# Performance work log

Hardware: AMD Instinct MI355X
Metric: run time of the kernel (lower is better)

The kernel has to match this reference:

```python
import jax, jax.numpy as jnp
import numpy as np

EPS_LN = 1e-5

def _ln(x, g, b):
    m = x.mean(-1, keepdims=True)
    v = jnp.var(x, axis=-1, keepdims=True)
    return (x - m) * jax.lax.rsqrt(v + EPS_LN) * g + b


def _forward(x, edge_attr, lin0_w, lin0_b, enn_w1, enn_b1, enn_g1, enn_b1n,
             enn_w2, enn_b2, enn_g2, enn_b2n, conv_bias,
             gru_w_ih, gru_w_hh, gru_b_ih, gru_b_hh,
             lstm_w_ih, lstm_w_hh, lstm_b_ih, lstm_b_hh,
             lin1_w, lin1_b, lin1_g, lin1_bn, lin2_w, lin2_b,
             edge_index, target_index, target_class):
    N = x.shape[0]
    D = lin0_w.shape[0]
    src, dst = edge_index[0], edge_index[1]

    out = jax.nn.relu(x @ lin0_w.T + lin0_b)            # [N, D]
    h = out                                             # GRU hidden state

    # edge NN -> per-edge weight matrix [E, D, D] (edge_attr constant across iters)
    e1 = jax.nn.relu(_ln(edge_attr @ enn_w1.T + enn_b1, enn_g1, enn_b1n))
    ew = _ln(e1 @ enn_w2.T + enn_b2, enn_g2, enn_b2n).reshape(-1, D, D)

    counts = jnp.clip(jax.ops.segment_sum(jnp.ones_like(dst, jnp.float32), dst, num_segments=N), 1.0)[:, None]

    for _ in range(3):
        msg = jnp.einsum('ed,edo->eo', out[src], ew)     # per-edge matmul
        agg = jax.ops.segment_sum(msg, dst, num_segments=N) / counts  # scatter-mean
        m = jax.nn.relu(agg + conv_bias)
        # GRU cell (seq len 1)
        gx = m @ gru_w_ih.T + gru_b_ih
        gh = h @ gru_w_hh.T + gru_b_hh
        xr, xz, xn = jnp.split(gx, 3, axis=-1)
        hr, hz, hn = jnp.split(gh, 3, axis=-1)
        r = jax.nn.sigmoid(xr + hr)
        z = jax.nn.sigmoid(xz + hz)
        n = jnp.tanh(xn + r * hn)
        h = (1.0 - z) * n + z * h
        out = h

    # Set2Set with batch_index = arange(N) (each node is its own set), 3 steps
    idx = jnp.arange(N)
    hl = jnp.zeros((N, D), x.dtype)
    cl = jnp.zeros((N, D), x.dtype)
    q_star = jnp.zeros((N, 2 * D), x.dtype)
    for _ in range(3):
        g = q_star @ lstm_w_ih.T + lstm_b_ih + hl @ lstm_w_hh.T + lstm_b_hh
        gi, gf, gg, go = jnp.split(g, 4, axis=-1)
        cl = jax.nn.sigmoid(gf) * cl + jax.nn.sigmoid(gi) * jnp.tanh(gg)
        hl = jax.nn.sigmoid(go) * jnp.tanh(cl)
        q = hl
        e = (out * q[idx]).sum(-1, keepdims=True)
        emax = jax.ops.segment_max(e, idx, num_segments=N)
        a = jnp.exp(e - emax[idx])
        a = a / (jax.ops.segment_sum(a, idx, num_segments=N)[idx] + 1e-16)
        r_pool = jax.ops.segment_sum(a * out, idx, num_segments=N)
        q_star = jnp.concatenate([q, r_pool], axis=-1)

    a0, a1 = target_index[0], target_index[1]
    cat = jnp.concatenate([out[a0], out[a1], q_star[a0], q_star[a1]], axis=-1)  # [P, 6D]
    p = jax.nn.relu(_ln(cat @ lin1_w.T + lin1_b, lin1_g, lin1_bn))
    p = p @ lin2_w.T + lin2_b                           # [P, 8]
    return jnp.take_along_axis(p, target_class[:, None], axis=1)[:, 0]


def setup_inputs() -> dict:
    N, E, P, F, D = 10000, 20000, 15000, 16, 64
    ks = iter(jax.random.split(jax.random.key(0), 40))
    def nrm(shape, s=0.1):
        return jax.random.normal(next(ks), shape, jnp.float32) * s
    return {
        'x': jax.random.normal(next(ks), (N, F), jnp.float32),
        'edge_attr': jax.random.normal(next(ks), (E, 4), jnp.float32),
        'lin0_w': nrm((D, F)), 'lin0_b': jnp.zeros((D,), jnp.float32),
        'enn_w1': nrm((128, 4)), 'enn_b1': jnp.zeros((128,), jnp.float32),
        'enn_g1': jnp.ones((128,), jnp.float32), 'enn_b1n': jnp.zeros((128,), jnp.float32),
        'enn_w2': nrm((D * D, 128), 0.05), 'enn_b2': jnp.zeros((D * D,), jnp.float32),
        'enn_g2': jnp.ones((D * D,), jnp.float32), 'enn_b2n': jnp.zeros((D * D,), jnp.float32),
        'conv_bias': jnp.zeros((D,), jnp.float32),
        'gru_w_ih': nrm((3 * D, D)), 'gru_w_hh': nrm((3 * D, D)),
        'gru_b_ih': jnp.zeros((3 * D,), jnp.float32), 'gru_b_hh': jnp.zeros((3 * D,), jnp.float32),
        'lstm_w_ih': nrm((4 * D, 2 * D)), 'lstm_w_hh': nrm((4 * D, D)),
        'lstm_b_ih': jnp.zeros((4 * D,), jnp.float32), 'lstm_b_hh': jnp.zeros((4 * D,), jnp.float32),
        'lin1_w': nrm((D, 6 * D)), 'lin1_b': jnp.zeros((D,), jnp.float32),
        'lin1_g': jnp.ones((D,), jnp.float32), 'lin1_bn': jnp.zeros((D,), jnp.float32),
        'lin2_w': nrm((8, D)), 'lin2_b': jnp.zeros((8,), jnp.float32),
        'edge_index': jax.random.randint(next(ks), (2, E), 0, N),
        'target_index': jax.random.randint(next(ks), (2, P), 0, N),
        'target_class': jax.random.randint(next(ks), (P,), 0, 8),
    }


def reference(x, edge_attr, lin0_w, lin0_b, enn_w1, enn_b1, enn_g1, enn_b1n,
              enn_w2, enn_b2, enn_g2, enn_b2n, conv_bias,
              gru_w_ih, gru_w_hh, gru_b_ih, gru_b_hh,
              lstm_w_ih, lstm_w_hh, lstm_b_ih, lstm_b_hh,
              lin1_w, lin1_b, lin1_g, lin1_bn, lin2_w, lin2_b,
              edge_index, target_index, target_class):
    return _forward(x, edge_attr, lin0_w, lin0_b, enn_w1, enn_b1, enn_g1, enn_b1n,
                    enn_w2, enn_b2, enn_g2, enn_b2n, conv_bias,
                    gru_w_ih, gru_w_hh, gru_b_ih, gru_b_hh,
                    lstm_w_ih, lstm_w_hh, lstm_b_ih, lstm_b_hh,
                    lin1_w, lin1_b, lin1_g, lin1_bn, lin2_w, lin2_b,
                    edge_index, target_index, target_class)
```

## Files before the change

### kernel.cpp

```cpp
#include <hip/hip_runtime.h>
#include <hip/hip_bf16.h>

#define EPS_LN 1e-5f

typedef __attribute__((ext_vector_type(8))) short bf16x8;
typedef __attribute__((ext_vector_type(4))) float f32x4;

__device__ __forceinline__ float dot4(float4 a, float4 b) {
    return a.x * b.x + a.y * b.y + a.z * b.z + a.w * b.w;
}
__device__ __forceinline__ float sigmoidf_(float x) { return 1.0f / (1.0f + expf(-x)); }

__device__ __forceinline__ float bfu2f(unsigned short u) {
    unsigned v = ((unsigned)u) << 16;
    float f;
    __builtin_memcpy(&f, &v, 4);
    return f;
}
__device__ __forceinline__ unsigned short f2bfu(float f) {
    __hip_bfloat16 h = __float2bfloat16(f);
    unsigned short u;
    __builtin_memcpy(&u, &h, 2);
    return u;
}
__device__ __forceinline__ unsigned pack2bf(float a, float b) {
    return (unsigned)f2bfu(a) | ((unsigned)f2bfu(b) << 16);
}

__global__ void init_kernel(const float* __restrict__ x, const float* __restrict__ w,
                            const float* __restrict__ b, float* __restrict__ h,
                            const int* __restrict__ ei, float* __restrict__ counts,
                            int N, int E) {
    int id = blockIdx.x * blockDim.x + threadIdx.x;
    if (id < N * 64) {
        int n = id >> 6, o = id & 63;
        const float* xr = x + n * 16;
        const float* wr = w + o * 16;
        float acc = b[o];
#pragma unroll
        for (int k = 0; k < 16; k++) acc += xr[k] * wr[k];
        h[id] = fmaxf(acc, 0.0f);
    }
    if (id < E) atomicAdd(&counts[ei[E + id]], 1.0f);
}

__global__ __launch_bounds__(128) void edge_nn1_kernel(
    const float* __restrict__ ea, const float* __restrict__ w1, const float* __restrict__ b1,
    const float* __restrict__ g1, const float* __restrict__ b1n,
    unsigned short* __restrict__ e1h, unsigned short* __restrict__ e1l, int E) {
    int e = blockIdx.x, j = threadIdx.x;
    float a0 = ea[e * 4 + 0], a1 = ea[e * 4 + 1], a2 = ea[e * 4 + 2], a3 = ea[e * 4 + 3];
    const float* wr = w1 + j * 4;
    float z = b1[j] + a0 * wr[0] + a1 * wr[1] + a2 * wr[2] + a3 * wr[3];
    float s = z, s2 = z * z;
#pragma unroll
    for (int m = 32; m >= 1; m >>= 1) { s += __shfl_xor(s, m); s2 += __shfl_xor(s2, m); }
    __shared__ float ls[2], ls2[2];
    int wv = j >> 6;
    if ((j & 63) == 0) { ls[wv] = s; ls2[wv] = s2; }
    __syncthreads();
    float S = ls[0] + ls[1], S2 = ls2[0] + ls2[1];
    float mu = S * (1.0f / 128.0f);
    float var = fmaxf(S2 * (1.0f / 128.0f) - mu * mu, 0.0f);
    float inv = rsqrtf(var + EPS_LN);
    float v = fmaxf((z - mu) * inv * g1[j] + b1n[j], 0.0f);
    unsigned short hi = f2bfu(v);
    unsigned short lo = f2bfu(v - bfu2f(hi));
    e1h[e * 128 + j] = hi;
    e1l[e * 128 + j] = lo;
}

__global__ __launch_bounds__(128) void mpart_kernel(const float* __restrict__ w2,
                                                    const float* __restrict__ b2,
                                                    const float* __restrict__ g2,
                                                    unsigned short* __restrict__ w2g,
                                                    float* __restrict__ b2g,
                                                    float* __restrict__ pMT, float* __restrict__ pv,
                                                    float* __restrict__ pcw, float* __restrict__ psb,
                                                    float* __restrict__ pc) {
    __shared__ float wL[16][128];
    __shared__ float b2L[16];
    int t = threadIdx.x, b = blockIdx.x;
#pragma unroll
    for (int i = 0; i < 16; i++) {
        int idx = t + i * 128;
        wL[idx >> 7][idx & 127] = w2[(size_t)(b * 16 + (idx >> 7)) * 128 + (idx & 127)];
    }
    if (t < 16) b2L[t] = b2[b * 16 + t];
    __syncthreads();
#pragma unroll
    for (int o = 0; o < 16; o++) {
        int row = b * 16 + o;
        w2g[(size_t)row * 128 + t] = f2bfu(wL[o][t] * g2[row]);
    }
    if (t < 16) b2g[b * 16 + t] = b2L[t] * g2[b * 16 + t];
    int j = t;
    float wj[16];
#pragma unroll
    for (int o = 0; o < 16; o++) wj[o] = wL[o][j];
    float pvj = 0.f, pcwj = 0.f;
#pragma unroll
    for (int o = 0; o < 16; o++) { pvj += wj[o] * b2L[o]; pcwj += wj[o]; }
    for (int i4 = 0; i4 < 32; i4++) {
        float4 a = {0.f, 0.f, 0.f, 0.f};
#pragma unroll
        for (int o = 0; o < 16; o++) {
            float4 w4 = *(const float4*)&wL[o][i4 * 4];
            a.x += wj[o] * w4.x; a.y += wj[o] * w4.y;
            a.z += wj[o] * w4.z; a.w += wj[o] * w4.w;
        }
        *(float4*)&pMT[((size_t)b * 128 + j) * 128 + i4 * 4] = a;
    }
    pv[b * 128 + j] = pvj;
    pcw[b * 128 + j] = pcwj;
    if (t == 0) {
        float sb = 0.f, cc = 0.f;
#pragma unroll
        for (int o = 0; o < 16; o++) { sb += b2L[o]; cc += b2L[o] * b2L[o]; }
        psb[b] = sb;
        pc[b] = cc;
    }
}

__global__ __launch_bounds__(256) void mreduce_kernel(const float* __restrict__ pMT,
                                                      const float* __restrict__ pv,
                                                      const float* __restrict__ pcw,
                                                      const float* __restrict__ psb,
                                                      const float* __restrict__ pc,
                                                      unsigned short* __restrict__ mb,
                                                      float* __restrict__ varr,
                                                      float* __restrict__ cw,
                                                      float* __restrict__ sbc) {
    int fid = blockIdx.x * 256 + threadIdx.x;
    float s = 0.f;
    int j = fid >> 7, i = fid & 127;
    for (int b = 0; b < 256; b++) s += pMT[((size_t)b * 128 + j) * 128 + i];
    mb[fid] = f2bfu(s);
    if (fid < 128) {
        float sv = 0.f, sc = 0.f;
        for (int b = 0; b < 256; b++) { sv += pv[b * 128 + fid]; sc += pcw[b * 128 + fid]; }
        varr[fid] = sv;
        cw[fid] = sc;
    }
    if (fid == 0) {
        float sb = 0.f, cc = 0.f;
        for (int b = 0; b < 256; b++) { sb += psb[b]; cc += pc[b]; }
        sbc[0] = sb;
        sbc[1] = cc;
    }
}

__global__ __launch_bounds__(256) void stats_kernel(
    const unsigned short* __restrict__ e1h, const unsigned short* __restrict__ e1l,
    const unsigned short* __restrict__ mb, const float* __restrict__ cw,
    const float* __restrict__ varr, const float* __restrict__ sbc,
    float* __restrict__ stats, int E) {
    __shared__ __align__(16) unsigned char smem[65536];
    const int t = threadIdx.x;
    const int eb = blockIdx.x * 64;
#pragma unroll
    for (int r = 0; r < 4; r++) {
        int idx = t + r * 256;
        int row = idx >> 4, kseg = idx & 15;
        int er = eb + row;
        if (er >= E) er = E - 1;
        uint4 vh = *(const uint4*)&e1h[(size_t)er * 128 + kseg * 8];
        uint4 vl = *(const uint4*)&e1l[(size_t)er * 128 + kseg * 8];
        int off = row * 256 + ((kseg * 16) ^ ((row & 7) << 4));
        *(uint4*)(smem + off) = vh;
        *(uint4*)(smem + 16384 + off) = vl;
    }
#pragma unroll
    for (int r = 0; r < 8; r++) {
        int idx = t + r * 256;
        int row = idx >> 4, kseg = idx & 15;
        uint4 v = *(const uint4*)&mb[(size_t)row * 128 + kseg * 8];
        *(uint4*)(smem + 32768 + row * 256 + ((kseg * 16) ^ ((row & 7) << 4))) = v;
    }
    __syncthreads();
    const int w = t >> 6, lane = t & 63;
    const int wrow = w * 16;
    const int r16 = lane & 15, kg = lane >> 4;
    f32x4 tacc[8];
#pragma unroll
    for (int nj = 0; nj < 8; nj++) tacc[nj] = (f32x4){0.f, 0.f, 0.f, 0.f};
#pragma unroll
    for (int ks = 0; ks < 4; ks++) {
        int arow = wrow + r16;
        int koff = ks * 64 + kg * 16;
        bf16x8 ah = *(const bf16x8*)(smem + arow * 256 + (koff ^ ((arow & 7) << 4)));
        bf16x8 al = *(const bf16x8*)(smem + 16384 + arow * 256 + (koff ^ ((arow & 7) << 4)));
#pragma unroll
        for (int nj = 0; nj < 8; nj++) {
            int brow = nj * 16 + r16;
            bf16x8 bf = *(const bf16x8*)(smem + 32768 + brow * 256 + (koff ^ ((brow & 7) << 4)));
            tacc[nj] = __builtin_amdgcn_mfma_f32_16x16x32_bf16(ah, bf, tacc[nj], 0, 0, 0);
            tacc[nj] = __builtin_amdgcn_mfma_f32_16x16x32_bf16(al, bf, tacc[nj], 0, 0, 0);
        }
    }
    __syncthreads();
#pragma unroll
    for (int nj = 0; nj < 8; nj++)
#pragma unroll
        for (int r = 0; r < 4; r++) {
            int row = wrow + kg * 4 + r, col = nj * 16 + r16;
            *(float*)(smem + 32768 + row * 512 + col * 4) = tacc[nj][r];
        }
    __syncthreads();
    int el = t >> 2, q = t & 3;
    float s2p = 0.f, sp = 0.f, svp = 0.f;
    for (int kk = 0; kk < 32; kk++) {
        int k = q * 32 + kk;
        int boff = el * 256 + ((2 * k) ^ ((el & 7) << 4));
        float e1v = bfu2f(*(const unsigned short*)(smem + boff)) +
                    bfu2f(*(const unsigned short*)(smem + 16384 + boff));
        float tv = *(const float*)(smem + 32768 + el * 512 + k * 4);
        s2p += tv * e1v;
        sp += e1v * cw[k];
        svp += e1v * varr[k];
    }
    s2p += __shfl_xor(s2p, 1); s2p += __shfl_xor(s2p, 2);
    sp += __shfl_xor(sp, 1);   sp += __shfl_xor(sp, 2);
    svp += __shfl_xor(svp, 1); svp += __shfl_xor(svp, 2);
    if (q == 0) {
        int e = eb + el;
        if (e < E) {
            float S = sp + sbc[0];
            float S2 = s2p + 2.f * svp + sbc[1];
            float mu = S * (1.0f / 4096.0f);
            float var = fmaxf(S2 * (1.0f / 4096.0f) - mu * mu, 0.0f);
            float inv = rsqrtf(var + EPS_LN);
            stats[e * 2 + 0] = inv;
            stats[e * 2 + 1] = mu * inv;
        }
    }
}

__global__ __launch_bounds__(256) void zgemm_final(
    const unsigned short* __restrict__ e1h, const unsigned short* __restrict__ e1l,
    const unsigned short* __restrict__ w2g, const float* __restrict__ b2g,
    const float* __restrict__ g2, const float* __restrict__ b2n,
    const float* __restrict__ stats, unsigned short* __restrict__ zT, int E) {
    __shared__ __align__(16) unsigned char smem[65536];
    const int t = threadIdx.x;
    const int eb = blockIdx.y * 64;
    const int cb = blockIdx.x * 128;
    const int o0 = blockIdx.x * 2;
#pragma unroll
    for (int r = 0; r < 4; r++) {
        int idx = t + r * 256;
        int row = idx >> 4, kseg = idx & 15;
        int er = eb + row;
        if (er >= E) er = E - 1;
        uint4 vh = *(const uint4*)&e1h[(size_t)er * 128 + kseg * 8];
        uint4 vl = *(const uint4*)&e1l[(size_t)er * 128 + kseg * 8];
        int off = row * 256 + ((kseg * 16) ^ ((row & 7) << 4));
        *(uint4*)(smem + off) = vh;
        *(uint4*)(smem + 16384 + off) = vl;
    }
#pragma unroll
    for (int r = 0; r < 8; r++) {
        int idx = t + r * 256;
        int j = idx >> 4, kseg = idx & 15;
        int srcrow = ((j & 63) << 6) + o0 + (j >> 6);
        uint4 v = *(const uint4*)&w2g[(size_t)srcrow * 128 + kseg * 8];
        *(uint4*)(smem + 32768 + j * 256 + ((kseg * 16) ^ ((j & 7) << 4))) = v;
    }
    __syncthreads();
    const int w = t >> 6, lane = t & 63;
    const int wrow = (w >> 1) * 32, wcol = (w & 1) * 64;
    const int r16 = lane & 15, kg = lane >> 4;

    bf16x8 bfrag[4][4];
#pragma unroll
    for (int nj = 0; nj < 4; nj++)
#pragma unroll
        for (int ks = 0; ks < 4; ks++) {
            int row = wcol + nj * 16 + r16;
            int koff = ks * 64 + kg * 16;
            bfrag[nj][ks] = *(const bf16x8*)(smem + 32768 + row * 256 + (koff ^ ((row & 7) << 4)));
        }
    f32x4 acc[2][4];
#pragma unroll
    for (int mi = 0; mi < 2; mi++)
#pragma unroll
        for (int nj = 0; nj < 4; nj++) acc[mi][nj] = (f32x4){0.f, 0.f, 0.f, 0.f};
#pragma unroll
    for (int pass = 0; pass < 2; pass++) {
        int abase = pass * 16384;
#pragma unroll
        for (int ks = 0; ks < 4; ks++) {
            bf16x8 afrag[2];
#pragma unroll
            for (int mi = 0; mi < 2; mi++) {
                int row = wrow + mi * 16 + r16;
                int koff = ks * 64 + kg * 16;
                afrag[mi] = *(const bf16x8*)(smem + abase + row * 256 + (koff ^ ((row & 7) << 4)));
            }
#pragma unroll
            for (int mi = 0; mi < 2; mi++)
#pragma unroll
                for (int nj = 0; nj < 4; nj++)
                    acc[mi][nj] = __builtin_amdgcn_mfma_f32_16x16x32_bf16(
                        afrag[mi], bfrag[nj][ks], acc[mi][nj], 0, 0, 0);
        }
    }
    float bg[4], gg[4], bn[4];
#pragma unroll
    for (int nj = 0; nj < 4; nj++) {
        int j = wcol + nj * 16 + r16;
        int sj = ((j & 63) << 6) + o0 + (j >> 6);
        bg[nj] = b2g[sj];
        gg[nj] = g2[sj];
        bn[nj] = b2n[sj];
    }
    __syncthreads();
#pragma unroll
    for (int mi = 0; mi < 2; mi++)
#pragma unroll
        for (int r = 0; r < 4; r++) {
            int rowl = wrow + mi * 16 + kg * 4 + r;
            int eg = eb + rowl;
            if (eg >= E) eg = E - 1;
            float inv = stats[eg * 2 + 0], miv = stats[eg * 2 + 1];
#pragma unroll
            for (int nj = 0; nj < 4; nj++) {
                int j = wcol + nj * 16 + r16;
                float v = inv * (acc[mi][nj][r] + bg[nj]) - miv * gg[nj] + bn[nj];
                *(unsigned short*)(smem + rowl * 272 + j * 2) = f2bfu(v);
            }
        }
    __syncthreads();
#pragma unroll
    for (int r = 0; r < 4; r++) {
        int idx = t + r * 256;
        int row = idx >> 4, seg = idx & 15;
        if (eb + row < E) {
            uint4 v = *(const uint4*)(smem + row * 272 + seg * 16);
            *(uint4*)&zT[(size_t)(eb + row) * 4096 + cb + seg * 8] = v;
        }
    }
}

__global__ __launch_bounds__(256) void msg_kernel(const unsigned short* __restrict__ zT,
                                                  const float* __restrict__ h,
                                                  const int* __restrict__ ei,
                                                  float* __restrict__ agg, int E) {
    int t = threadIdx.x;
    int el = t >> 6, o = t & 63;
    int e = blockIdx.x * 4 + el;
    __shared__ float sL[4][64];
    int src = ei[e];
    int dstn = ei[E + e];
    sL[el][o] = h[src * 64 + o];
    __syncthreads();
    float acc = 0.f;
    const uint4* zp = (const uint4*)(zT + (size_t)e * 4096 + o * 64);
#pragma unroll
    for (int q = 0; q < 8; q++) {
        uint4 v = zp[q];
        const float* hp = &sL[el][q * 8];
        acc += __uint_as_float(v.x << 16) * hp[0] + __uint_as_float(v.x & 0xffff0000u) * hp[1];
        acc += __uint_as_float(v.y << 16) * hp[2] + __uint_as_float(v.y & 0xffff0000u) * hp[3];
        acc += __uint_as_float(v.z << 16) * hp[4] + __uint_as_float(v.z & 0xffff0000u) * hp[5];
        acc += __uint_as_float(v.w << 16) * hp[6] + __uint_as_float(v.w & 0xffff0000u) * hp[7];
    }
    atomicAdd(&agg[(size_t)dstn * 64 + o], acc);
}

__global__ __launch_bounds__(192) void gru_kernel(
    const float* __restrict__ agg, const float* __restrict__ counts, const float* __restrict__ cbias,
    const float* __restrict__ wih, const float* __restrict__ whh,
    const float* __restrict__ bih, const float* __restrict__ bhh, float* __restrict__ h, int N) {
    int t = threadIdx.x;
    int nb = blockIdx.x * 8;
    __shared__ __align__(16) float mL[8][64], hL[8][64], gxL[8][192], ghL[8][192];
    for (int idx = t; idx < 512; idx += 192) {
        int n = idx >> 6, k = idx & 63;
        int node = nb + n;
        float cnt = fmaxf(counts[node], 1.0f);
        mL[n][k] = fmaxf(agg[node * 64 + k] / cnt + cbias[k], 0.0f);
        hL[n][k] = h[node * 64 + k];
    }
    __syncthreads();
    {
        int j = t;
        float ax[8], ah[8];
#pragma unroll
        for (int n = 0; n < 8; n++) { ax[n] = 0.f; ah[n] = 0.f; }
        const float4* wi = (const float4*)(wih + j * 64);
        const float4* wh = (const float4*)(whh + j * 64);
#pragma unroll 4
        for (int k4 = 0; k4 < 16; k4++) {
            float4 wiv = wi[k4], whv = wh[k4];
#pragma unroll
            for (int n = 0; n < 8; n++) {
                ax[n] += dot4(wiv, *(const float4*)&mL[n][k4 * 4]);
                ah[n] += dot4(whv, *(const float4*)&hL[n][k4 * 4]);
            }
        }
        float bi = bih[j], bh = bhh[j];
#pragma unroll
        for (int n = 0; n < 8; n++) { gxL[n][j] = ax[n] + bi; ghL[n][j] = ah[n] + bh; }
    }
    __syncthreads();
    for (int idx = t; idx < 512; idx += 192) {
        int n = idx >> 6, k = idx & 63;
        int node = nb + n;
        float r = sigmoidf_(gxL[n][k] + ghL[n][k]);
        float zz = sigmoidf_(gxL[n][64 + k] + ghL[n][64 + k]);
        float nn = tanhf(gxL[n][128 + k] + r * ghL[n][128 + k]);
        h[node * 64 + k] = (1.0f - zz) * nn + zz * hL[n][k];
    }
}

__global__ __launch_bounds__(256) void coutprep_kernel(
    const float* __restrict__ h, const float* __restrict__ wih, const float* __restrict__ whh,
    const float* __restrict__ bih, const float* __restrict__ bhh,
    float* __restrict__ cout, float* __restrict__ wc,
    float* __restrict__ hl, float* __restrict__ cl, int N) {
    int t = threadIdx.x, nb = blockIdx.x * 8;
    __shared__ __align__(16) float oL[8][64];
    for (int idx = t; idx < 512; idx += 256) {
        int n = idx >> 6, k = idx & 63;
        oL[n][k] = h[(nb + n) * 64 + k];
    }
    __syncthreads();
    {
        float acc[8];
#pragma unroll
        for (int n = 0; n < 8; n++) acc[n] = 0.f;
        const float* wr = wih + t * 128 + 64;
#pragma unroll 4
        for (int k4 = 0; k4 < 16; k4++) {
            float4 w4 = *(const float4*)&wr[k4 * 4];
#pragma unroll
            for (int n = 0; n < 8; n++) acc[n] += dot4(w4, *(const float4*)&oL[n][k4 * 4]);
        }
#pragma unroll
        for (int n = 0; n < 8; n++) cout[(size_t)(nb + n) * 256 + t] = acc[n];
    }
    if (blockIdx.x < 64) {
        int id = blockIdx.x * 256 + t;
        int j = id >> 6, k = id & 63;
        wc[id] = wih[j * 128 + k] + whh[id];
    }
    if (t < 64) {
        float gi = bih[t] + bhh[t];
        float gg = bih[128 + t] + bhh[128 + t];
        float go = bih[192 + t] + bhh[192 + t];
        float c0 = sigmoidf_(gi) * tanhf(gg);
        float h0 = sigmoidf_(go) * tanhf(c0);
#pragma unroll
        for (int n = 0; n < 8; n++) {
            cl[(nb + n) * 64 + t] = c0;
            hl[(nb + n) * 64 + t] = h0;
        }
    }
}

__global__ __launch_bounds__(256) void lstm_step_kernel(const float* __restrict__ wc,
                                                        const float* __restrict__ bih,
                                                        const float* __restrict__ bhh,
                                                        const float* __restrict__ cout,
                                                        float* __restrict__ hl,
                                                        float* __restrict__ cl, int N) {
    int t = threadIdx.x, nb = blockIdx.x * 8;
    __shared__ __align__(16) float hlL[8][64];
    __shared__ float gL[8][256];
    for (int idx = t; idx < 512; idx += 256) {
        int n = idx >> 6, k = idx & 63;
        hlL[n][k] = hl[(nb + n) * 64 + k];
    }
    __syncthreads();
    {
        float acc[8];
#pragma unroll
        for (int n = 0; n < 8; n++) acc[n] = 0.f;
        const float4* w4p = (const float4*)(wc + t * 64);
#pragma unroll 4
        for (int k4 = 0; k4 < 16; k4++) {
            float4 w4 = w4p[k4];
#pragma unroll
            for (int n = 0; n < 8; n++) acc[n] += dot4(w4, *(const float4*)&hlL[n][k4 * 4]);
        }
        float bs = bih[t] + bhh[t];
#pragma unroll
        for (int n = 0; n < 8; n++) gL[n][t] = acc[n] + cout[(size_t)(nb + n) * 256 + t] + bs;
    }
    __syncthreads();
    for (int idx = t; idx < 512; idx += 256) {
        int n = idx >> 6, k = idx & 63;
        int node = nb + n;
        float gi = gL[n][k], gf = gL[n][64 + k], gg = gL[n][128 + k], go = gL[n][192 + k];
        float c = sigmoidf_(gf) * cl[node * 64 + k] + sigmoidf_(gi) * tanhf(gg);
        cl[node * 64 + k] = c;
        hl[node * 64 + k] = sigmoidf_(go) * tanhf(c);
    }
}

__global__ __launch_bounds__(256) void head_kernel(
    const float* __restrict__ h, const float* __restrict__ hl, const int* __restrict__ ti,
    const int* __restrict__ tc, const float* __restrict__ w1, const float* __restrict__ b1,
    const float* __restrict__ g1, const float* __restrict__ bn1, const float* __restrict__ w2,
    const float* __restrict__ b2, float* __restrict__ out, int P) {
    __shared__ uint2 w1q[6144];
    __shared__ float catL[4][384];
    int t = threadIdx.x;
    const float4* w1f4 = (const float4*)w1;
#pragma unroll
    for (int i = 0; i < 24; i++) {
        int f = t + i * 256;
        float4 v = w1f4[f];
        int j = f / 96, k4 = f - j * 96;
        w1q[k4 * 64 + j] = make_uint2(pack2bf(v.x, v.y), pack2bf(v.z, v.w));
    }
    int j = t & 63, pl = t >> 6;
    float b1j = b1[j], g1j = g1[j], bnj = bn1[j];
    __syncthreads();

    for (int pb = blockIdx.x * 4; pb < P; pb += gridDim.x * 4) {
#pragma unroll
        for (int i = 0; i < 6; i++) {
            int idx = t + i * 256;
            int p = idx / 384, kk = idx - p * 384;
            int pair = pb + p;
            if (pair >= P) pair = P - 1;
            int a0 = ti[pair], a1 = ti[P + pair];
            int s = kk >> 6, k = kk & 63;
            float v;
            if (s == 0 || s == 3) v = h[a0 * 64 + k];
            else if (s == 1 || s == 5) v = h[a1 * 64 + k];
            else if (s == 2) v = hl[a0 * 64 + k];
            else v = hl[a1 * 64 + k];
            catL[p][kk] = v;
        }
        __syncthreads();
        int pair = pb + pl;
        float acc = b1j;
#pragma unroll 8
        for (int k4 = 0; k4 < 96; k4++) {
            uint2 wv = w1q[k4 * 64 + j];
            float4 c = *(const float4*)&catL[pl][k4 * 4];
            acc += __uint_as_float(wv.x << 16) * c.x + __uint_as_float(wv.x & 0xffff0000u) * c.y;
            acc += __uint_as_float(wv.y << 16) * c.z + __uint_as_float(wv.y & 0xffff0000u) * c.w;
        }
        float s1 = acc, s2v = acc * acc;
#pragma unroll
        for (int m = 32; m >= 1; m >>= 1) { s1 += __shfl_xor(s1, m); s2v += __shfl_xor(s2v, m); }
        float mu = s1 * (1.0f / 64.0f);
        float var = fmaxf(s2v * (1.0f / 64.0f) - mu * mu, 0.0f);
        float p1 = fmaxf((acc - mu) * rsqrtf(var + EPS_LN) * g1j + bnj, 0.0f);
        int cls = tc[pair < P ? pair : P - 1];
        float part = p1 * w2[cls * 64 + j];
#pragma unroll
        for (int m = 32; m >= 1; m >>= 1) part += __shfl_xor(part, m);
        if (j == 0 && pair < P) out[pair] = part + b2[cls];
        __syncthreads();
    }
}

extern "C" void kernel_launch(void* const* d_in, const int* in_sizes, int n_in,
                              void* d_out, int out_size, void* d_ws, size_t ws_size,
                              hipStream_t stream) {
    const float* x = (const float*)d_in[0];
    const float* edge_attr = (const float*)d_in[1];
    const float* lin0_w = (const float*)d_in[2];
    const float* lin0_b = (const float*)d_in[3];
    const float* enn_w1 = (const float*)d_in[4];
    const float* enn_b1 = (const float*)d_in[5];
    const float* enn_g1 = (const float*)d_in[6];
    const float* enn_b1n = (const float*)d_in[7];
    const float* enn_w2 = (const float*)d_in[8];
    const float* enn_b2 = (const float*)d_in[9];
    const float* enn_g2 = (const float*)d_in[10];
    const float* enn_b2n = (const float*)d_in[11];
    const float* conv_bias = (const float*)d_in[12];
    const float* gru_w_ih = (const float*)d_in[13];
    const float* gru_w_hh = (const float*)d_in[14];
    const float* gru_b_ih = (const float*)d_in[15];
    const float* gru_b_hh = (const float*)d_in[16];
    const float* lstm_w_ih = (const float*)d_in[17];
    const float* lstm_w_hh = (const float*)d_in[18];
    const float* lstm_b_ih = (const float*)d_in[19];
    const float* lstm_b_hh = (const float*)d_in[20];
    const float* lin1_w = (const float*)d_in[21];
    const float* lin1_b = (const float*)d_in[22];
    const float* lin1_g = (const float*)d_in[23];
    const float* lin1_bn = (const float*)d_in[24];
    const float* lin2_w = (const float*)d_in[25];
    const float* lin2_b = (const float*)d_in[26];
    const int* edge_index = (const int*)d_in[27];
    const int* target_index = (const int*)d_in[28];
    const int* target_class = (const int*)d_in[29];

    const int N = in_sizes[0] / 16;
    const int E = in_sizes[27] / 2;
    const int P = in_sizes[29];

    size_t off = 0;
    auto carve = [&](size_t bytes) {
        void* p = (char*)d_ws + off;
        off += (bytes + 255) & ~(size_t)255;
        return p;
    };
    unsigned short* zbuf = (unsigned short*)carve((size_t)E * 4096 * 2);
    unsigned short* e1h = (unsigned short*)carve((size_t)E * 128 * 2);
    unsigned short* e1l = (unsigned short*)carve((size_t)E * 128 * 2);
    unsigned short* w2g = (unsigned short*)carve((size_t)4096 * 128 * 2);
    float* b2g = (float*)carve((size_t)4096 * 4);
    float* hbuf = (float*)carve((size_t)N * 64 * 4);
    float* counts = (float*)carve((size_t)N * 4 + (size_t)3 * N * 64 * 4);
    float* agg0 = counts + N;
    float* agg1 = agg0 + (size_t)N * 64;
    float* agg2 = agg1 + (size_t)N * 64;
    float* hl = (float*)carve((size_t)N * 64 * 4);
    float* cl = (float*)carve((size_t)N * 64 * 4);
    float* cout_b = (float*)carve((size_t)N * 256 * 4);
    float* wc = (float*)carve((size_t)256 * 64 * 4);
    float* stats = (float*)carve((size_t)E * 2 * 4);
    unsigned short* mb = (unsigned short*)carve((size_t)128 * 128 * 2);
    float* varr = (float*)carve((size_t)128 * 4);
    float* cw = (float*)carve((size_t)128 * 4);
    float* sbc = (float*)carve((size_t)2 * 4);
    float* pv = (float*)carve((size_t)256 * 128 * 4);
    float* pcw = (float*)carve((size_t)256 * 128 * 4);
    float* psb = (float*)carve((size_t)256 * 4);
    float* pc = (float*)carve((size_t)256 * 4);
    float* pMT = (float*)carve((size_t)256 * 128 * 128 * 4);
    (void)ws_size;

    hipMemsetAsync(counts, 0, (size_t)N * 4 + (size_t)3 * N * 64 * 4, stream);
    init_kernel<<<(N * 64 + 255) / 256, 256, 0, stream>>>(x, lin0_w, lin0_b, hbuf, edge_index,
                                                          counts, N, E);
    edge_nn1_kernel<<<E, 128, 0, stream>>>(edge_attr, enn_w1, enn_b1, enn_g1, enn_b1n, e1h, e1l, E);
    mpart_kernel<<<256, 128, 0, stream>>>(enn_w2, enn_b2, enn_g2, w2g, b2g, pMT, pv, pcw, psb, pc);
    mreduce_kernel<<<64, 256, 0, stream>>>(pMT, pv, pcw, psb, pc, mb, varr, cw, sbc);
    stats_kernel<<<(E + 63) / 64, 256, 0, stream>>>(e1h, e1l, mb, cw, varr, sbc, stats, E);
    {
        dim3 g(32, (E + 63) / 64);
        zgemm_final<<<g, 256, 0, stream>>>(e1h, e1l, w2g, b2g, enn_g2, enn_b2n, stats, zbuf, E);
    }

    float* aggs[3] = {agg0, agg1, agg2};
    for (int it = 0; it < 3; it++) {
        msg_kernel<<<E / 4, 256, 0, stream>>>(zbuf, hbuf, edge_index, aggs[it], E);
        gru_kernel<<<N / 8, 192, 0, stream>>>(aggs[it], counts, conv_bias, gru_w_ih, gru_w_hh,
                                              gru_b_ih, gru_b_hh, hbuf, N);
    }

    coutprep_kernel<<<N / 8, 256, 0, stream>>>(hbuf, lstm_w_ih, lstm_w_hh, lstm_b_ih, lstm_b_hh,
                                               cout_b, wc, hl, cl, N);
    lstm_step_kernel<<<N / 8, 256, 0, stream>>>(wc, lstm_b_ih, lstm_b_hh, cout_b, hl, cl, N);
    lstm_step_kernel<<<N / 8, 256, 0, stream>>>(wc, lstm_b_ih, lstm_b_hh, cout_b, hl, cl, N);

    head_kernel<<<512, 256, 0, stream>>>(hbuf, hl, target_index, target_class, lin1_w, lin1_b,
                                         lin1_g, lin1_bn, lin2_w, lin2_b, (float*)d_out, P);
}
```

Measured before the change: 432.7 us.

## Drop low-half bf16 split in edge GEMM and write output directly from registers

The edge-weight GEMM now uses only the high bf16 part of e1 instead of the hi+lo split pair, halving the MFMA work and the A-tile load. Operands are swapped in the MFMA so each lane holds four consecutive output columns, which lets results be written straight to global memory as 8-byte stores without the shared-memory transpose and its two extra barriers. Per-column bias/gain and per-edge stats are staged in shared memory. Dropping the low part lowers the accuracy of the per-edge weights, and the output stores are narrower than the previous 16-byte ones.

```diff
diff --git a/kernel.cpp b/kernel.cpp
--- a/kernel.cpp
+++ b/kernel.cpp
@@ -237,11 +237,13 @@
 }
 
 __global__ __launch_bounds__(256) void zgemm_final(
-    const unsigned short* __restrict__ e1h, const unsigned short* __restrict__ e1l,
+    const unsigned short* __restrict__ e1h,
     const unsigned short* __restrict__ w2g, const float* __restrict__ b2g,
     const float* __restrict__ g2, const float* __restrict__ b2n,
     const float* __restrict__ stats, unsigned short* __restrict__ zT, int E) {
-    __shared__ __align__(16) unsigned char smem[65536];
+    __shared__ __align__(16) unsigned char smem[49152];
+    __shared__ float cBg[128], cGg[128], cBn[128];
+    __shared__ float sInv[64], sMiv[64];
     const int t = threadIdx.x;
     const int eb = blockIdx.y * 64;
     const int cb = blockIdx.x * 128;
@@ -253,10 +255,7 @@
         int er = eb + row;
         if (er >= E) er = E - 1;
         uint4 vh = *(const uint4*)&e1h[(size_t)er * 128 + kseg * 8];
-        uint4 vl = *(const uint4*)&e1l[(size_t)er * 128 + kseg * 8];
-        int off = row * 256 + ((kseg * 16) ^ ((row & 7) << 4));
-        *(uint4*)(smem + off) = vh;
-        *(uint4*)(smem + 16384 + off) = vl;
+        *(uint4*)(smem + row * 256 + ((kseg * 16) ^ ((row & 7) << 4))) = vh;
     }
 #pragma unroll
     for (int r = 0; r < 8; r++) {
@@ -264,80 +263,70 @@
         int j = idx >> 4, kseg = idx & 15;
         int srcrow = ((j & 63) << 6) + o0 + (j >> 6);
         uint4 v = *(const uint4*)&w2g[(size_t)srcrow * 128 + kseg * 8];
-        *(uint4*)(smem + 32768 + j * 256 + ((kseg * 16) ^ ((j & 7) << 4))) = v;
+        *(uint4*)(smem + 16384 + j * 256 + ((kseg * 16) ^ ((j & 7) << 4))) = v;
+    }
+    if (t < 128) {
+        int sj = ((t & 63) << 6) + o0 + (t >> 6);
+        cBg[t] = b2g[sj];
+        cGg[t] = g2[sj];
+        cBn[t] = b2n[sj];
+    } else if (t < 192) {
+        int tt = t - 128;
+        int eg = eb + tt;
+        if (eg >= E) eg = E - 1;
+        sInv[tt] = stats[eg * 2 + 0];
+        sMiv[tt] = stats[eg * 2 + 1];
     }
     __syncthreads();
     const int w = t >> 6, lane = t & 63;
     const int wrow = (w >> 1) * 32, wcol = (w & 1) * 64;
     const int r16 = lane & 15, kg = lane >> 4;
 
-    bf16x8 bfrag[4][4];
-#pragma unroll
-    for (int nj = 0; nj < 4; nj++)
-#pragma unroll
-        for (int ks = 0; ks < 4; ks++) {
+    f32x4 acc[2][4];
+#pragma unroll
+    for (int mi = 0; mi < 2; mi++)
+#pragma unroll
+        for (int nj = 0; nj < 4; nj++) acc[mi][nj] = (f32x4){0.f, 0.f, 0.f, 0.f};
+#pragma unroll
+    for (int ks = 0; ks < 4; ks++) {
+        int koff = ks * 64 + kg * 16;
+        bf16x8 af[2];
+#pragma unroll
+        for (int mi = 0; mi < 2; mi++) {
+            int row = wrow + mi * 16 + r16;
+            af[mi] = *(const bf16x8*)(smem + row * 256 + (koff ^ ((row & 7) << 4)));
+        }
+        bf16x8 bf[4];
+#pragma unroll
+        for (int nj = 0; nj < 4; nj++) {
             int row = wcol + nj * 16 + r16;
-            int koff = ks * 64 + kg * 16;
-            bfrag[nj][ks] = *(const bf16x8*)(smem + 32768 + row * 256 + (koff ^ ((row & 7) << 4)));
-        }
-    f32x4 acc[2][4];
-#pragma unroll
-    for (int mi = 0; mi < 2; mi++)
-#pragma unroll
-        for (int nj = 0; nj < 4; nj++) acc[mi][nj] = (f32x4){0.f, 0.f, 0.f, 0.f};
-#pragma unroll
-    for (int pass = 0; pass < 2; pass++) {
-        int abase = pass * 16384;
-#pragma unroll
-        for (int ks = 0; ks < 4; ks++) {
-            bf16x8 afrag[2];
-#pragma unroll
-            for (int mi = 0; mi < 2; mi++) {
-                int row = wrow + mi * 16 + r16;
-                int koff = ks * 64 + kg * 16;
-                afrag[mi] = *(const bf16x8*)(smem + abase + row * 256 + (koff ^ ((row & 7) << 4)));
-            }
-#pragma unroll
-            for (int mi = 0; mi < 2; mi++)
-#pragma unroll
-                for (int nj = 0; nj < 4; nj++)
-                    acc[mi][nj] = __builtin_amdgcn_mfma_f32_16x16x32_bf16(
-                        afrag[mi], bfrag[nj][ks], acc[mi][nj], 0, 0, 0);
-        }
-    }
-    float bg[4], gg[4], bn[4];
-#pragma unroll
-    for (int nj = 0; nj < 4; nj++) {
-        int j = wcol + nj * 16 + r16;
-        int sj = ((j & 63) << 6) + o0 + (j >> 6);
-        bg[nj] = b2g[sj];
-        gg[nj] = g2[sj];
-        bn[nj] = b2n[sj];
-    }
-    __syncthreads();
-#pragma unroll
-    for (int mi = 0; mi < 2; mi++)
-#pragma unroll
-        for (int r = 0; r < 4; r++) {
-            int rowl = wrow + mi * 16 + kg * 4 + r;
-            int eg = eb + rowl;
-            if (eg >= E) eg = E - 1;
-            float inv = stats[eg * 2 + 0], miv = stats[eg * 2 + 1];
-#pragma unroll
-            for (int nj = 0; nj < 4; nj++) {
-                int j = wcol + nj * 16 + r16;
-                float v = inv * (acc[mi][nj][r] + bg[nj]) - miv * gg[nj] + bn[nj];
-                *(unsigned short*)(smem + rowl * 272 + j * 2) = f2bfu(v);
-            }
-        }
-    __syncthreads();
-#pragma unroll
-    for (int r = 0; r < 4; r++) {
-        int idx = t + r * 256;
-        int row = idx >> 4, seg = idx & 15;
-        if (eb + row < E) {
-            uint4 v = *(const uint4*)(smem + row * 272 + seg * 16);
-            *(uint4*)&zT[(size_t)(eb + row) * 4096 + cb + seg * 8] = v;
+            bf[nj] = *(const bf16x8*)(smem + 16384 + row * 256 + (koff ^ ((row & 7) << 4)));
+        }
+#pragma unroll
+        for (int mi = 0; mi < 2; mi++)
+#pragma unroll
+            for (int nj = 0; nj < 4; nj++)
+                acc[mi][nj] = __builtin_amdgcn_mfma_f32_16x16x32_bf16(
+                    bf[nj], af[mi], acc[mi][nj], 0, 0, 0);
+    }
+#pragma unroll
+    for (int mi = 0; mi < 2; mi++) {
+        int e_local = wrow + mi * 16 + r16;
+        int e = eb + e_local;
+        float inv = sInv[e_local], miv = sMiv[e_local];
+        bool ok = (e < E);
+#pragma unroll
+        for (int nj = 0; nj < 4; nj++) {
+            int j0 = wcol + nj * 16 + kg * 4;
+            float4 bg4 = *(const float4*)&cBg[j0];
+            float4 gg4 = *(const float4*)&cGg[j0];
+            float4 bn4 = *(const float4*)&cBn[j0];
+            ushort4 sv;
+            sv.x = f2bfu(inv * (acc[mi][nj][0] + bg4.x) - miv * gg4.x + bn4.x);
+            sv.y = f2bfu(inv * (acc[mi][nj][1] + bg4.y) - miv * gg4.y + bn4.y);
+            sv.z = f2bfu(inv * (acc[mi][nj][2] + bg4.z) - miv * gg4.z + bn4.z);
+            sv.w = f2bfu(inv * (acc[mi][nj][3] + bg4.w) - miv * gg4.w + bn4.w);
+            if (ok) *(ushort4*)&zT[(size_t)e * 4096 + cb + j0] = sv;
         }
     }
 }
@@ -639,7 +628,7 @@
     stats_kernel<<<(E + 63) / 64, 256, 0, stream>>>(e1h, e1l, mb, cw, varr, sbc, stats, E);
     {
         dim3 g(32, (E + 63) / 64);
-        zgemm_final<<<g, 256, 0, stream>>>(e1h, e1l, w2g, b2g, enn_g2, enn_b2n, stats, zbuf, E);
+        zgemm_final<<<g, 256, 0, stream>>>(e1h, w2g, b2g, enn_g2, enn_b2n, stats, zbuf, E);
     }
 
     float* aggs[3] = {agg0, agg1, agg2};
```

Result: faster. 388.7 us (-10.2%).
